# Optimization experiments

Measured on AMD Instinct MI355X. Metric: run time of the kernel, lower is better.

Reference implementation:

```python
import jax, jax.numpy as jnp
import numpy as np

N_NODES = 20000
N_EDGES = 640000
IN_DIM = 128
HID = 128
NUM_GRAPHS = 64


def setup_inputs() -> dict:
    key = jax.random.key(0)
    ks = jax.random.split(key, 12)
    x = jax.random.normal(ks[0], (N_NODES, IN_DIM), dtype=jnp.float32)
    edge_index = jax.random.randint(ks[1], (2, N_EDGES), 0, N_NODES, dtype=jnp.int64)
    batch = jnp.sort(jax.random.randint(ks[2], (N_NODES,), 0, NUM_GRAPHS, dtype=jnp.int64))
    edge_attr = jax.random.uniform(ks[3], (N_EDGES,), dtype=jnp.float32)
    s1 = 1.0 / np.sqrt(IN_DIM)
    s2 = 1.0 / np.sqrt(HID)
    # GraphConv layer 1: lin_rel (with bias) on aggregated messages, lin_root (no bias) on x
    W1_rel = jax.random.uniform(ks[4], (HID, IN_DIM), minval=-s1, maxval=s1, dtype=jnp.float32)
    b1 = jax.random.uniform(ks[5], (HID,), minval=-s1, maxval=s1, dtype=jnp.float32)
    W1_root = jax.random.uniform(ks[6], (HID, IN_DIM), minval=-s1, maxval=s1, dtype=jnp.float32)
    # GraphConv layer 3 (conv2 is unused in forward)
    W3_rel = jax.random.uniform(ks[7], (HID, HID), minval=-s2, maxval=s2, dtype=jnp.float32)
    b3 = jax.random.uniform(ks[8], (HID,), minval=-s2, maxval=s2, dtype=jnp.float32)
    W3_root = jax.random.uniform(ks[9], (HID, HID), minval=-s2, maxval=s2, dtype=jnp.float32)
    # Final linear head
    Wlin = jax.random.uniform(ks[10], (1, HID), minval=-s2, maxval=s2, dtype=jnp.float32)
    blin = jax.random.uniform(ks[11], (1,), minval=-s2, maxval=s2, dtype=jnp.float32)
    return {
        "x": x, "edge_index": edge_index, "batch": batch, "edge_attr": edge_attr,
        "W1_rel": W1_rel, "b1": b1, "W1_root": W1_root,
        "W3_rel": W3_rel, "b3": b3, "W3_root": W3_root,
        "Wlin": Wlin, "blin": blin, "num_graphs": NUM_GRAPHS,
    }


def graph_conv(x, src, dst, edge_w, W_rel, b_rel, W_root):
    # PyG GraphConv (aggr='add'): out = W_rel @ sum_{j in N(i)} w_ij * x_j + b_rel + W_root @ x_i
    msg = x[src] * edge_w[:, None]                       # [E, d] gather + scale
    agg = jax.ops.segment_sum(msg, dst, num_segments=x.shape[0])  # [N, d] scatter-add
    return agg @ W_rel.T + b_rel + x @ W_root.T


def reference(x, edge_index, batch, edge_attr,
              W1_rel, b1, W1_root, W3_rel, b3, W3_root, Wlin, blin, num_graphs):
    src, dst = edge_index[0], edge_index[1]
    h = graph_conv(x, src, dst, edge_attr, W1_rel, b1, W1_root)
    h = jax.nn.relu(h)
    # dropout p=0.5 is identity in eval mode
    h = graph_conv(h, src, dst, edge_attr, W3_rel, b3, W3_root)
    # global_mean_pool over per-node graph ids
    sums = jax.ops.segment_sum(h, batch, num_segments=num_graphs)          # [G, H]
    counts = jax.ops.segment_sum(jnp.ones((h.shape[0],), h.dtype), batch,
                                 num_segments=num_graphs)                  # [G]
    pooled = sums / jnp.maximum(counts, 1.0)[:, None]
    out = jax.nn.relu(pooled @ Wlin.T + blin)                              # [G, 1]
    return out
```

## Files before the change

### kernel.cpp

```cpp
#include <hip/hip_runtime.h>

#define N_NODES 20000
#define N_EDGES 640000
#define DIM 128
#define NGRAPH 64
#define NBUCK 313
#define EPB 2048
#define NB_GEMM 1252
#define NB_HIST 313
#define RED_BLOCKS 512

__global__ __launch_bounds__(256, 2) void k_front(
    const float* __restrict__ x, const float* __restrict__ Wrel,
    const float* __restrict__ Wroot, const float* __restrict__ b1,
    float* __restrict__ y, float* __restrict__ r,
    const int* __restrict__ dst,
    int* __restrict__ ghist, int* __restrict__ ticket_hist,
    int* __restrict__ boff, int* __restrict__ gcursor,
    const float* __restrict__ W3rel, const float* __restrict__ W3root,
    const float* __restrict__ b3, const float* __restrict__ Wlin,
    float* __restrict__ vrel, float* __restrict__ vroot, float* __restrict__ cb3) {

    __shared__ float sA[64][132];
    __shared__ float sB[64][132];
    __shared__ int lhist[NBUCK];
    __shared__ int islast;

    const int t = threadIdx.x;
    const int blk = blockIdx.x;

    if (blk < NB_GEMM) {
        const int node0 = (blk % 313) * 64;
        const int col0 = (blk / 313) * 64;

        for (int ch = 0; ch < 8; ++ch) {
            int idx = ch * 256 + t;
            int row = idx >> 5;
            int k4 = idx & 31;
            int gn = node0 + row;
            float4 v = make_float4(0.f, 0.f, 0.f, 0.f);
            if (gn < N_NODES) v = ((const float4*)x)[gn * 32 + k4];
            *(float4*)&sA[row][k4 * 4] = v;
        }
        for (int ch = 0; ch < 8; ++ch) {
            int idx = ch * 256 + t;
            int c = idx >> 5;
            int k4 = idx & 31;
            int gc = col0 + c;
            const float* srcw = (gc < DIM) ? (Wrel + gc * DIM) : (Wroot + (gc - DIM) * DIM);
            float4 v = ((const float4*)srcw)[k4];
            *(float4*)&sB[c][k4 * 4] = v;
        }
        __syncthreads();

        const int tr = (t >> 4) * 4;
        const int tc = (t & 15) * 4;
        float acc[4][4] = {};
        for (int k = 0; k < DIM; k += 4) {
            float4 a[4], b[4];
            for (int i = 0; i < 4; ++i) a[i] = *(const float4*)&sA[tr + i][k];
            for (int j = 0; j < 4; ++j) b[j] = *(const float4*)&sB[tc + j][k];
            for (int i = 0; i < 4; ++i)
                for (int j = 0; j < 4; ++j)
                    acc[i][j] = fmaf(a[i].x, b[j].x,
                                fmaf(a[i].y, b[j].y,
                                fmaf(a[i].z, b[j].z,
                                fmaf(a[i].w, b[j].w, acc[i][j]))));
        }
        for (int i = 0; i < 4; ++i) {
            int gn = node0 + tr + i;
            if (gn >= N_NODES) continue;
            int gc = col0 + tc;
            if (gc < DIM) {
                *(float4*)&y[gn * DIM + gc] =
                    make_float4(acc[i][0], acc[i][1], acc[i][2], acc[i][3]);
            } else {
                int c = gc - DIM;
                *(float4*)&r[gn * DIM + c] =
                    make_float4(acc[i][0] + b1[c], acc[i][1] + b1[c + 1],
                                acc[i][2] + b1[c + 2], acc[i][3] + b1[c + 3]);
            }
        }
    } else if (blk < NB_GEMM + NB_HIST) {
        const int hb = blk - NB_GEMM;
        for (int i = t; i < NBUCK; i += 256) lhist[i] = 0;
        __syncthreads();
        const int e0 = hb * EPB;
        for (int i = 0; i < 8; ++i) {
            int e = e0 + i * 256 + t;
            if (e < N_EDGES) atomicAdd(&lhist[dst[e] >> 6], 1);
        }
        __syncthreads();
        for (int i = t; i < NBUCK; i += 256)
            if (lhist[i]) atomicAdd(&ghist[i], lhist[i]);
        __syncthreads();
        if (t == 0) {
            __threadfence();
            int old = atomicAdd(ticket_hist, 1);
            islast = (old == NB_HIST - 1);
        }
        __syncthreads();
        if (islast) {
            __threadfence();
            if (t < 64) {
                int carry = 0;
                for (int c = 0; c < 5; ++c) {
                    int idx = c * 64 + t;
                    int v = (idx < NBUCK)
                        ? __hip_atomic_load(&ghist[idx], __ATOMIC_RELAXED,
                                            __HIP_MEMORY_SCOPE_AGENT)
                        : 0;
                    int xv = v;
                    for (int s = 1; s < 64; s <<= 1) {
                        int u = __shfl_up(xv, s);
                        if (t >= s) xv += u;
                    }
                    int excl = carry + xv - v;
                    if (idx < NBUCK) { boff[idx] = excl; gcursor[idx] = excl; }
                    carry += __shfl(xv, 63);
                }
                if (t == 0) boff[NBUCK] = carry;
            }
        }
    } else {
        if (t < 64) {
            for (int kk = 0; kk < 2; ++kk) {
                int k = t + kk * 64;
                float sr = 0.f, so = 0.f;
                for (int h = 0; h < DIM; ++h) {
                    float wl = Wlin[h];
                    sr = fmaf(wl, W3rel[h * DIM + k], sr);
                    so = fmaf(wl, W3root[h * DIM + k], so);
                }
                vrel[k] = sr;
                vroot[k] = so;
            }
            float c = b3[t] * Wlin[t] + b3[t + 64] * Wlin[t + 64];
            for (int m = 32; m > 0; m >>= 1) c += __shfl_xor(c, m);
            if (t == 0) cb3[0] = c;
        }
    }
}

__global__ __launch_bounds__(256) void k_partition(const int* __restrict__ src,
                                                   const int* __restrict__ dst,
                                                   const float* __restrict__ ew,
                                                   int* __restrict__ gcursor,
                                                   int2* __restrict__ part) {
    __shared__ int lhist[NBUCK], gbase[NBUCK], lcur[NBUCK];
    const int t = threadIdx.x;
    for (int i = t; i < NBUCK; i += 256) lhist[i] = 0;
    __syncthreads();
    const int e0 = blockIdx.x * EPB;
    int mys[8], myd[8];
    float myw[8];
    for (int i = 0; i < 8; ++i) {
        int e = e0 + i * 256 + t;
        if (e < N_EDGES) {
            mys[i] = src[e];
            myd[i] = dst[e];
            myw[i] = ew[e];
            atomicAdd(&lhist[myd[i] >> 6], 1);
        } else {
            myd[i] = -1;
        }
    }
    __syncthreads();
    for (int i = t; i < NBUCK; i += 256) {
        gbase[i] = lhist[i] ? atomicAdd(&gcursor[i], lhist[i]) : 0;
        lcur[i] = 0;
    }
    __syncthreads();
    for (int i = 0; i < 8; ++i) {
        if (myd[i] >= 0) {
            int b = myd[i] >> 6;
            int rk = atomicAdd(&lcur[b], 1);
            part[gbase[b] + rk] =
                make_int2(((myd[i] & 63) << 16) | mys[i], __float_as_int(myw[i]));
        }
    }
}

__global__ __launch_bounds__(256) void k_bucketsort(const int* __restrict__ boff,
                                                    const int2* __restrict__ part,
                                                    int2* __restrict__ sorted,
                                                    int* __restrict__ off) {
    __shared__ int nh[64], ncur[64];
    const int b = blockIdx.x;
    const int t = threadIdx.x;
    const int s0 = boff[b], s1 = boff[b + 1];
    if (t < 64) nh[t] = 0;
    __syncthreads();
    for (int i = s0 + t; i < s1; i += 256) atomicAdd(&nh[part[i].x >> 16], 1);
    __syncthreads();
    if (t < 64) {
        int v = nh[t];
        int xv = v;
        for (int s = 1; s < 64; s <<= 1) {
            int u = __shfl_up(xv, s);
            if (t >= s) xv += u;
        }
        int excl = xv - v;
        ncur[t] = excl;
        int node = b * 64 + t;
        if (node < N_NODES) off[node] = s0 + excl;
    }
    __syncthreads();
    for (int i = s0 + t; i < s1; i += 256) {
        int2 rc = part[i];
        int dl = rc.x >> 16;
        int p = atomicAdd(&ncur[dl], 1);
        sorted[s0 + p] = make_int2(rc.x & 0xFFFF, rc.y);
    }
    if (b == 0 && t == 0) off[N_NODES] = N_EDGES;
}

__global__ __launch_bounds__(256) void k_agg(const float2* __restrict__ y2,
                                             const float2* __restrict__ r2,
                                             const int* __restrict__ off,
                                             const int2* __restrict__ grec,
                                             const float2* __restrict__ vrel2,
                                             const float2* __restrict__ vroot2,
                                             float* __restrict__ aout,
                                             float* __restrict__ bout) {
    const int lane = threadIdx.x & 63;
    const int node = blockIdx.x * 4 + (threadIdx.x >> 6);
    if (node >= N_NODES) return;

    int j = off[node];
    const int e1 = off[node + 1];
    float sx = 0.f, sy = 0.f;
    for (; j + 4 <= e1; j += 4) {
        int2 r0 = grec[j], r1 = grec[j + 1], rr2 = grec[j + 2], r3 = grec[j + 3];
        float w0 = __int_as_float(r0.y), w1 = __int_as_float(r1.y);
        float w2 = __int_as_float(rr2.y), w3 = __int_as_float(r3.y);
        float2 v0 = y2[r0.x * 64 + lane];
        float2 v1 = y2[r1.x * 64 + lane];
        float2 v2 = y2[rr2.x * 64 + lane];
        float2 v3 = y2[r3.x * 64 + lane];
        sx = fmaf(w0, v0.x, fmaf(w1, v1.x, fmaf(w2, v2.x, fmaf(w3, v3.x, sx))));
        sy = fmaf(w0, v0.y, fmaf(w1, v1.y, fmaf(w2, v2.y, fmaf(w3, v3.y, sy))));
    }
    for (; j < e1; ++j) {
        int2 rc = grec[j];
        float w = __int_as_float(rc.y);
        float2 v = y2[rc.x * 64 + lane];
        sx = fmaf(w, v.x, sx);
        sy = fmaf(w, v.y, sy);
    }
    float2 rr = r2[node * 64 + lane];
    float hx = fmaxf(sx + rr.x, 0.f);
    float hy = fmaxf(sy + rr.y, 0.f);
    float2 vr = vrel2[lane];
    float2 vo = vroot2[lane];
    float pa = hx * vr.x + hy * vr.y;
    float pb = hx * vo.x + hy * vo.y;
    for (int m = 32; m > 0; m >>= 1) {
        pa += __shfl_xor(pa, m);
        pb += __shfl_xor(pb, m);
    }
    if (lane == 0) {
        aout[node] = pa;
        bout[node] = pb;
    }
}

__global__ __launch_bounds__(256) void k_reduce_final(
    const int2* __restrict__ sorted, const int* __restrict__ off,
    const float* __restrict__ a, const float* __restrict__ bvec,
    const int* __restrict__ batch,
    float* __restrict__ gpart, int* __restrict__ gpartc,
    int* __restrict__ ticket_red,
    const float* __restrict__ cb3, const float* __restrict__ blin,
    float* __restrict__ out) {
    __shared__ float sbin[NGRAPH];
    __shared__ int cbin[NGRAPH];
    __shared__ int islast;
    const int t = threadIdx.x;
    for (int i = t; i < NGRAPH; i += 256) { sbin[i] = 0.f; cbin[i] = 0; }
    __syncthreads();
    const int lane = t & 63;
    const int gw = blockIdx.x * 4 + (t >> 6);
    const int nw = gridDim.x * 4;
    for (int node = gw; node < N_NODES; node += nw) {
        const int e0 = off[node], e1 = off[node + 1];
        float s = 0.f;
        for (int j = e0 + lane; j < e1; j += 64) {
            int2 rc = sorted[j];
            s = fmaf(__int_as_float(rc.y), a[rc.x], s);
        }
        for (int m = 32; m > 0; m >>= 1) s += __shfl_xor(s, m);
        if (lane == 0) {
            int g = batch[node];
            atomicAdd(&sbin[g], s + bvec[node]);
            atomicAdd(&cbin[g], 1);
        }
    }
    __syncthreads();
    const int slot = blockIdx.x & 63;
    for (int i = t; i < NGRAPH; i += 256) {
        atomicAdd(&gpart[slot * NGRAPH + i], sbin[i]);
        if (cbin[i]) atomicAdd(&gpartc[slot * NGRAPH + i], cbin[i]);
    }
    __syncthreads();
    if (t == 0) {
        __threadfence();
        islast = (atomicAdd(ticket_red, 1) == (int)gridDim.x - 1);
    }
    __syncthreads();
    if (islast) {
        __threadfence();
        if (t < NGRAPH) {
            float S = 0.f;
            int C = 0;
            for (int s2 = 0; s2 < 64; ++s2) {
                S += __hip_atomic_load(&gpart[s2 * NGRAPH + t], __ATOMIC_RELAXED,
                                       __HIP_MEMORY_SCOPE_AGENT);
                C += __hip_atomic_load(&gpartc[s2 * NGRAPH + t], __ATOMIC_RELAXED,
                                       __HIP_MEMORY_SCOPE_AGENT);
            }
            float denom = (C > 0) ? (float)C : 1.f;
            float v = (S + (float)C * cb3[0]) / denom + blin[0];
            out[t] = (v > 0.f) ? v : 0.f;
        }
    }
}

extern "C" void kernel_launch(void* const* d_in, const int* in_sizes, int n_in,
                              void* d_out, int out_size, void* d_ws, size_t ws_size,
                              hipStream_t stream) {
    const float* x = (const float*)d_in[0];
    const int* edge_index = (const int*)d_in[1];
    const int* src = edge_index;
    const int* dst = edge_index + N_EDGES;
    const int* batch = (const int*)d_in[2];
    const float* ew = (const float*)d_in[3];
    const float* W1rel = (const float*)d_in[4];
    const float* b1 = (const float*)d_in[5];
    const float* W1root = (const float*)d_in[6];
    const float* W3rel = (const float*)d_in[7];
    const float* b3 = (const float*)d_in[8];
    const float* W3root = (const float*)d_in[9];
    const float* Wlin = (const float*)d_in[10];
    const float* blin = (const float*)d_in[11];
    float* out = (float*)d_out;

    char* w = (char*)d_ws;
    size_t o = 0;
    auto alloc = [&](size_t bytes) -> void* {
        void* p = w + o;
        o += bytes;
        o = (o + 255) & ~(size_t)255;
        return p;
    };
    char* zbase = (char*)alloc(1280 + 64 * NGRAPH * 4 * 2);
    int* ghist = (int*)zbase;
    int* ticket_hist = ghist + NBUCK;
    int* ticket_red = ghist + NBUCK + 1;
    float* gpart = (float*)(zbase + 1280);
    int* gpartc = (int*)(zbase + 1280 + 64 * NGRAPH * 4);
    const size_t zbytes = 1280 + 64 * NGRAPH * 4 * 2;

    float* y = (float*)alloc((size_t)N_NODES * DIM * 4);
    float* r = (float*)alloc((size_t)N_NODES * DIM * 4);
    int* boff = (int*)alloc((size_t)(NBUCK + 1) * 4);
    int* gcursor = (int*)alloc((size_t)NBUCK * 4);
    int2* part = (int2*)alloc((size_t)N_EDGES * 8);
    int2* sorted = (int2*)alloc((size_t)N_EDGES * 8);
    int* off = (int*)alloc((size_t)(N_NODES + 1) * 4);
    float* a = (float*)alloc((size_t)N_NODES * 4);
    float* b = (float*)alloc((size_t)N_NODES * 4);
    float* vrel = (float*)alloc(DIM * 4);
    float* vroot = (float*)alloc(DIM * 4);
    float* cb3 = (float*)alloc(4);

    hipMemsetAsync(zbase, 0, zbytes, stream);

    k_front<<<NB_GEMM + NB_HIST + 1, 256, 0, stream>>>(
        x, W1rel, W1root, b1, y, r, dst, ghist, ticket_hist, boff, gcursor,
        W3rel, W3root, b3, Wlin, vrel, vroot, cb3);

    k_partition<<<NB_HIST, 256, 0, stream>>>(src, dst, ew, gcursor, part);

    k_bucketsort<<<NBUCK, 256, 0, stream>>>(boff, part, sorted, off);

    k_agg<<<(N_NODES + 3) / 4, 256, 0, stream>>>(
        (const float2*)y, (const float2*)r, off, sorted,
        (const float2*)vrel, (const float2*)vroot, a, b);

    k_reduce_final<<<RED_BLOCKS, 256, 0, stream>>>(
        sorted, off, a, b, batch, gpart, gpartc, ticket_red, cb3, blin, out);
}
```

Before: 214.7 us.

## Store projected neighbor features as bf16 and swizzle GEMM weight tile in LDS

The per-node projection y = x·W1_rel^T is now rounded to bf16 when written and unpacked back to fp32 in the edge aggregation kernel. This halves the bytes gathered per edge, which is the dominant memory traffic. The front GEMM also XOR-swizzles the weight tile in shared memory to reduce LDS bank conflicts on the B-operand reads. The cost is reduced precision in the aggregated messages, which may shift results within bf16 tolerance.

```diff
diff --git a/kernel.cpp b/kernel.cpp
--- a/kernel.cpp
+++ b/kernel.cpp
@@ -10,10 +10,15 @@
 #define NB_HIST 313
 #define RED_BLOCKS 512
 
+__device__ __forceinline__ unsigned int bf16rne(float f) {
+    unsigned int u = __float_as_uint(f);
+    return (u + 0x7FFFu + ((u >> 16) & 1u)) >> 16;
+}
+
 __global__ __launch_bounds__(256, 2) void k_front(
     const float* __restrict__ x, const float* __restrict__ Wrel,
     const float* __restrict__ Wroot, const float* __restrict__ b1,
-    float* __restrict__ y, float* __restrict__ r,
+    unsigned int* __restrict__ yb, float* __restrict__ r,
     const int* __restrict__ dst,
     int* __restrict__ ghist, int* __restrict__ ticket_hist,
     int* __restrict__ boff, int* __restrict__ gcursor,
@@ -49,17 +54,21 @@
             int gc = col0 + c;
             const float* srcw = (gc < DIM) ? (Wrel + gc * DIM) : (Wroot + (gc - DIM) * DIM);
             float4 v = ((const float4*)srcw)[k4];
-            *(float4*)&sB[c][k4 * 4] = v;
+            int swk = k4 ^ ((c >> 2) & 7);
+            *(float4*)&sB[c][swk * 4] = v;
         }
         __syncthreads();
 
         const int tr = (t >> 4) * 4;
         const int tc = (t & 15) * 4;
+        const int u7 = t & 7;
         float acc[4][4] = {};
-        for (int k = 0; k < DIM; k += 4) {
+        for (int k4 = 0; k4 < 32; ++k4) {
+            const int k = k4 * 4;
+            const int swk = (k4 ^ u7) * 4;
             float4 a[4], b[4];
             for (int i = 0; i < 4; ++i) a[i] = *(const float4*)&sA[tr + i][k];
-            for (int j = 0; j < 4; ++j) b[j] = *(const float4*)&sB[tc + j][k];
+            for (int j = 0; j < 4; ++j) b[j] = *(const float4*)&sB[tc + j][swk];
             for (int i = 0; i < 4; ++i)
                 for (int j = 0; j < 4; ++j)
                     acc[i][j] = fmaf(a[i].x, b[j].x,
@@ -72,8 +81,10 @@
             if (gn >= N_NODES) continue;
             int gc = col0 + tc;
             if (gc < DIM) {
-                *(float4*)&y[gn * DIM + gc] =
-                    make_float4(acc[i][0], acc[i][1], acc[i][2], acc[i][3]);
+                uint2 p;
+                p.x = bf16rne(acc[i][0]) | (bf16rne(acc[i][1]) << 16);
+                p.y = bf16rne(acc[i][2]) | (bf16rne(acc[i][3]) << 16);
+                *(uint2*)&yb[gn * 64 + (gc >> 1)] = p;
             } else {
                 int c = gc - DIM;
                 *(float4*)&r[gn * DIM + c] =
@@ -215,7 +226,7 @@
     if (b == 0 && t == 0) off[N_NODES] = N_EDGES;
 }
 
-__global__ __launch_bounds__(256) void k_agg(const float2* __restrict__ y2,
+__global__ __launch_bounds__(256) void k_agg(const unsigned int* __restrict__ yb,
                                              const float2* __restrict__ r2,
                                              const int* __restrict__ off,
                                              const int2* __restrict__ grec,
@@ -234,19 +245,25 @@
         int2 r0 = grec[j], r1 = grec[j + 1], rr2 = grec[j + 2], r3 = grec[j + 3];
         float w0 = __int_as_float(r0.y), w1 = __int_as_float(r1.y);
         float w2 = __int_as_float(rr2.y), w3 = __int_as_float(r3.y);
-        float2 v0 = y2[r0.x * 64 + lane];
-        float2 v1 = y2[r1.x * 64 + lane];
-        float2 v2 = y2[rr2.x * 64 + lane];
-        float2 v3 = y2[r3.x * 64 + lane];
-        sx = fmaf(w0, v0.x, fmaf(w1, v1.x, fmaf(w2, v2.x, fmaf(w3, v3.x, sx))));
-        sy = fmaf(w0, v0.y, fmaf(w1, v1.y, fmaf(w2, v2.y, fmaf(w3, v3.y, sy))));
+        unsigned int v0 = yb[r0.x * 64 + lane];
+        unsigned int v1 = yb[r1.x * 64 + lane];
+        unsigned int v2 = yb[rr2.x * 64 + lane];
+        unsigned int v3 = yb[r3.x * 64 + lane];
+        sx = fmaf(w0, __uint_as_float(v0 << 16),
+             fmaf(w1, __uint_as_float(v1 << 16),
+             fmaf(w2, __uint_as_float(v2 << 16),
+             fmaf(w3, __uint_as_float(v3 << 16), sx))));
+        sy = fmaf(w0, __uint_as_float(v0 & 0xFFFF0000u),
+             fmaf(w1, __uint_as_float(v1 & 0xFFFF0000u),
+             fmaf(w2, __uint_as_float(v2 & 0xFFFF0000u),
+             fmaf(w3, __uint_as_float(v3 & 0xFFFF0000u), sy))));
     }
     for (; j < e1; ++j) {
         int2 rc = grec[j];
         float w = __int_as_float(rc.y);
-        float2 v = y2[rc.x * 64 + lane];
-        sx = fmaf(w, v.x, sx);
-        sy = fmaf(w, v.y, sy);
+        unsigned int v = yb[rc.x * 64 + lane];
+        sx = fmaf(w, __uint_as_float(v << 16), sx);
+        sy = fmaf(w, __uint_as_float(v & 0xFFFF0000u), sy);
     }
     float2 rr = r2[node * 64 + lane];
     float hx = fmaxf(sx + rr.x, 0.f);
@@ -361,7 +378,7 @@
     int* gpartc = (int*)(zbase + 1280 + 64 * NGRAPH * 4);
     const size_t zbytes = 1280 + 64 * NGRAPH * 4 * 2;
 
-    float* y = (float*)alloc((size_t)N_NODES * DIM * 4);
+    unsigned int* yb = (unsigned int*)alloc((size_t)N_NODES * DIM * 2);
     float* r = (float*)alloc((size_t)N_NODES * DIM * 4);
     int* boff = (int*)alloc((size_t)(NBUCK + 1) * 4);
     int* gcursor = (int*)alloc((size_t)NBUCK * 4);
@@ -377,7 +394,7 @@
     hipMemsetAsync(zbase, 0, zbytes, stream);
 
     k_front<<<NB_GEMM + NB_HIST + 1, 256, 0, stream>>>(
-        x, W1rel, W1root, b1, y, r, dst, ghist, ticket_hist, boff, gcursor,
+        x, W1rel, W1root, b1, yb, r, dst, ghist, ticket_hist, boff, gcursor,
         W3rel, W3root, b3, Wlin, vrel, vroot, cb3);
 
     k_partition<<<NB_HIST, 256, 0, stream>>>(src, dst, ew, gcursor, part);
@@ -385,7 +402,7 @@
     k_bucketsort<<<NBUCK, 256, 0, stream>>>(boff, part, sorted, off);
 
     k_agg<<<(N_NODES + 3) / 4, 256, 0, stream>>>(
-        (const float2*)y, (const float2*)r, off, sorted,
+        yb, (const float2*)r, off, sorted,
         (const float2*)vrel, (const float2*)vroot, a, b);
 
     k_reduce_final<<<RED_BLOCKS, 256, 0, stream>>>(
```

Result: faster. 197.5 us (-8.0%).
